# Performance work log

Hardware: AMD Instinct MI355X
Metric: run time of the kernel (lower is better)

## Reference

```python
import jax, jax.numpy as jnp
import numpy as np

ALPHA = 0.5
BETA = 5.0
LOGIT_SCALE = 100.0  # exp(log(100)) -- CLIP's learned logit scale at its clamp value
NUM_CLASSES = 200


def _l2norm(x):
    return x / jnp.linalg.norm(x, axis=-1, keepdims=True)


def setup_inputs() -> dict:
    key = jax.random.key(0)
    k1, k2, k3, k4 = jax.random.split(key, 4)
    img_f = jax.random.normal(k1, (1024, 512), dtype=jnp.float32)
    text_features = jax.random.normal(k2, (200, 512), dtype=jnp.float32)
    keys = jax.random.normal(k3, (50000, 512), dtype=jnp.float32)
    labels = jax.random.randint(k4, (50000,), 0, NUM_CLASSES, dtype=jnp.int64)
    return {"img_f": img_f, "text_features": text_features, "keys": keys, "labels": labels}


def reference(img_f, text_features, keys, labels):
    # encode_image output is L2-normalized in the module; keys were built from
    # normalized image features, text_features are normalized class embeddings.
    q = _l2norm(img_f)            # [B, D]
    t = _l2norm(text_features)    # [C, D]
    k = _l2norm(keys)             # [N, D]

    # CLIP zero-shot branch: scale * q @ t.T -> [B, C]
    z = LOGIT_SCALE * jnp.einsum('bd,cd->bc', q, t)

    # Tip-Adapter cache branch: exp(beta * q @ keys.T) @ one_hot(labels)
    sim = jnp.einsum('bd,nd->bn', q, k)                 # [B, N]
    aff = jnp.exp(BETA * sim)                           # [B, N]
    values = jax.nn.one_hot(labels, NUM_CLASSES, dtype=aff.dtype)  # [N, C]
    c = aff @ values                                    # [B, C]

    return (1.0 - ALPHA) * z + ALPHA * c
```

## Files before the change

### kernel.cpp

```cpp
#include <hip/hip_runtime.h>

#define B_Q    1024
#define D_K    512
#define N_CLS  200
#define N_KEYS 50000
#define N_PAD  50048

typedef __attribute__((ext_vector_type(8))) short bf16x8;
typedef __attribute__((ext_vector_type(4))) float f32x4;

__device__ __forceinline__ float bf2f(unsigned short u) {
  union { unsigned int i; float f; } v; v.i = ((unsigned int)u) << 16; return v.f;
}
__device__ __forceinline__ unsigned short f2bf(float f) {
  union { float f; unsigned int i; } v; v.f = f;
  unsigned int r = v.i + 0x7fffu + ((v.i >> 16) & 1u);
  return (unsigned short)(r >> 16);
}
__device__ __forceinline__ uint4 pack8(const float f[8], float s) {
  uint4 o;
  o.x = (unsigned)f2bf(f[0]*s) | ((unsigned)f2bf(f[1]*s) << 16);
  o.y = (unsigned)f2bf(f[2]*s) | ((unsigned)f2bf(f[3]*s) << 16);
  o.z = (unsigned)f2bf(f[4]*s) | ((unsigned)f2bf(f[5]*s) << 16);
  o.w = (unsigned)f2bf(f[6]*s) | ((unsigned)f2bf(f[7]*s) << 16);
  return o;
}
__device__ __forceinline__ void async_copy16(const void* g, void* lds) {
  __builtin_amdgcn_global_load_lds(
      (const __attribute__((address_space(1))) unsigned int*)g,
      (__attribute__((address_space(3))) unsigned int*)lds, 16, 0, 0);
}

__global__ void k_hist(const int* __restrict__ labels, int* __restrict__ hist) {
  __shared__ int h[N_CLS];
  int t = threadIdx.x;
  if (t < N_CLS) h[t] = 0;
  __syncthreads();
  int n = blockIdx.x * 256 + t;
  if (n < N_KEYS) atomicAdd(&h[labels[n]], 1);
  __syncthreads();
  if (t < N_CLS && h[t]) atomicAdd(&hist[t], h[t]);
}

__global__ void k_scan(const int* __restrict__ hist, int* __restrict__ cursor) {
  __shared__ int s[N_CLS];
  int t = threadIdx.x;
  int v = (t < N_CLS) ? hist[t] : 0;
  if (t < N_CLS) s[t] = v;
  __syncthreads();
  for (int d = 1; d < N_CLS; d <<= 1) {
    int x = 0;
    if (t < N_CLS && t >= d) x = s[t - d];
    __syncthreads();
    if (t < N_CLS) s[t] += x;
    __syncthreads();
  }
  if (t < N_CLS) cursor[t] = s[t] - v;
}

__global__ void k_perm(const int* __restrict__ labels, int* __restrict__ cursor,
                       int* __restrict__ perm, int* __restrict__ cls) {
  __shared__ int lh[N_CLS];
  __shared__ int lbase[N_CLS];
  int t = threadIdx.x;
  if (t < N_CLS) lh[t] = 0;
  __syncthreads();
  int n = blockIdx.x * 256 + t;
  bool valid = (n < N_KEYS);
  int l = 0, lo = 0;
  if (valid) { l = labels[n]; lo = atomicAdd(&lh[l], 1); }
  __syncthreads();
  if (t < N_CLS && lh[t] > 0) lbase[t] = atomicAdd(&cursor[t], lh[t]);
  __syncthreads();
  if (valid) {
    int pos = lbase[l] + lo;
    perm[pos] = n;
    cls[pos] = l;
  } else if (n < N_PAD) {
    cls[n] = N_CLS;
  }
}

__global__ void k_norm2(const float* __restrict__ img, const float* __restrict__ txt,
                        unsigned short* __restrict__ qn, unsigned short* __restrict__ tn) {
  int w = threadIdx.x >> 6, lane = threadIdx.x & 63;
  int row = blockIdx.x * 4 + w;
  const float* in; unsigned short* out; int r;
  if (row < B_Q)                { in = img; out = qn; r = row; }
  else if (row < B_Q + N_CLS)   { in = txt; out = tn; r = row - B_Q; }
  else return;
  const float4* src = (const float4*)(in + (size_t)r * D_K) + lane * 2;
  float4 a = src[0], b = src[1];
  float f[8] = {a.x, a.y, a.z, a.w, b.x, b.y, b.z, b.w};
  float ss = 0.f;
#pragma unroll
  for (int i = 0; i < 8; i++) ss += f[i] * f[i];
#pragma unroll
  for (int d = 1; d < 64; d <<= 1) ss += __shfl_xor(ss, d);
  float rinv = rsqrtf(ss);
  *((uint4*)(out + (size_t)r * D_K) + lane) = pack8(f, rinv);
}

__global__ void k_prep(const float* __restrict__ keys,
                       const int* __restrict__ perm, unsigned short* __restrict__ kn) {
  int w = threadIdx.x >> 6, lane = threadIdx.x & 63;
  int j = blockIdx.x * 4 + w;
  if (j >= N_PAD) return;
  uint4* dst = (uint4*)(kn + (size_t)j * D_K) + lane;
  if (j >= N_KEYS) { *dst = make_uint4(0, 0, 0, 0); return; }
  int n = perm[j];
  const float4* src = (const float4*)(keys + (size_t)n * D_K) + lane * 2;
  float4 a = src[0], b = src[1];
  float f[8] = {a.x, a.y, a.z, a.w, b.x, b.y, b.z, b.w};
  float ss = 0.f;
#pragma unroll
  for (int i = 0; i < 8; i++) ss += f[i] * f[i];
#pragma unroll
  for (int d = 1; d < 64; d <<= 1) ss += __shfl_xor(ss, d);
  float rinv = rsqrtf(ss);
  *dst = pack8(f, rinv);
}

__global__ void k_z(const unsigned short* __restrict__ qn,
                    const unsigned short* __restrict__ tn, float* __restrict__ out) {
  __shared__ float qrow[D_K];
  int t = threadIdx.x, b = blockIdx.x;
  qrow[t]       = bf2f(qn[b * D_K + t]);
  qrow[t + 256] = bf2f(qn[b * D_K + 256 + t]);
  __syncthreads();
  if (t < N_CLS) {
    const uint4* trow = (const uint4*)(tn + (size_t)t * D_K);
    float s = 0.f;
    for (int k8 = 0; k8 < D_K / 8; k8++) {
      uint4 v = trow[k8];
      unsigned short h[8] = {
        (unsigned short)(v.x & 0xffffu), (unsigned short)(v.x >> 16),
        (unsigned short)(v.y & 0xffffu), (unsigned short)(v.y >> 16),
        (unsigned short)(v.z & 0xffffu), (unsigned short)(v.z >> 16),
        (unsigned short)(v.w & 0xffffu), (unsigned short)(v.w >> 16)};
      const float* qp = &qrow[k8 * 8];
#pragma unroll
      for (int i = 0; i < 8; i++) s += bf2f(h[i]) * qp[i];
    }
    out[b * N_CLS + t] = 50.0f * s;
  }
}

__global__ __launch_bounds__(256, 3) void k_main(const unsigned short* __restrict__ qn,
                                                 const unsigned short* __restrict__ kn,
                                                 const int* __restrict__ cls,
                                                 float* __restrict__ out) {
  __shared__ unsigned short As[128 * 64];
  __shared__ unsigned short Bs[128 * 64];
  int t = threadIdx.x;
  int tileB = blockIdx.x, tileN = blockIdx.y;
  int rowB0 = tileB * 128, rowN0 = tileN * 128;

  f32x4 acc[4][4];
#pragma unroll
  for (int i = 0; i < 4; i++)
#pragma unroll
    for (int j = 0; j < 4; j++) acc[i][j] = (f32x4){0.f, 0.f, 0.f, 0.f};

  int lane = t & 63, w = t >> 6;
  int wr = (w >> 1) * 64, wc = (w & 1) * 64;
  int l15 = lane & 15, lq = lane >> 4;
  const int rA = t >> 3;
  const int gsw = ((t & 7) ^ (rA & 7)) * 8;
  const int sw = l15 & 7;

  for (int k0 = 0; k0 < D_K; k0 += 64) {
    __syncthreads();
#pragma unroll
    for (int i = 0; i < 4; i++) {
      int row = i * 32 + rA;
      async_copy16(qn + (size_t)(rowB0 + row) * D_K + k0 + gsw, &As[i * 2048 + t * 8]);
      async_copy16(kn + (size_t)(rowN0 + row) * D_K + k0 + gsw, &Bs[i * 2048 + t * 8]);
    }
    __syncthreads();
#pragma unroll
    for (int ks = 0; ks < 64; ks += 32) {
      bf16x8 af[4], bf[4];
#pragma unroll
      for (int i = 0; i < 4; i++)
        af[i] = *(const bf16x8*)&As[(wr + 16 * i + l15) * 64 + ((((ks >> 3) + lq) ^ sw) * 8)];
#pragma unroll
      for (int j = 0; j < 4; j++)
        bf[j] = *(const bf16x8*)&Bs[(wc + 16 * j + l15) * 64 + ((((ks >> 3) + lq) ^ sw) * 8)];
#pragma unroll
      for (int i = 0; i < 4; i++)
#pragma unroll
        for (int j = 0; j < 4; j++)
          acc[i][j] = __builtin_amdgcn_mfma_f32_16x16x32_bf16(af[i], bf[j], acc[i][j], 0, 0, 0);
    }
  }

#pragma unroll
  for (int i = 0; i < 4; i++)
#pragma unroll
    for (int j = 0; j < 4; j++)
#pragma unroll
      for (int r = 0; r < 4; r++) acc[i][j][r] = __expf(5.0f * acc[i][j][r]);

  int cj[4];
#pragma unroll
  for (int j = 0; j < 4; j++) cj[j] = cls[rowN0 + wc + 16 * j + l15];
  int cseg0 = cls[rowN0 + wc];
  int cseg1 = cls[rowN0 + wc + 63];

  for (int c = cseg0; c <= cseg1; c++) {
    if (c >= N_CLS) break;
#pragma unroll
    for (int i = 0; i < 4; i++) {
      float s0 = 0.f, s1 = 0.f, s2 = 0.f, s3 = 0.f;
#pragma unroll
      for (int j = 0; j < 4; j++) {
        if (cj[j] == c) {
          s0 += acc[i][j][0]; s1 += acc[i][j][1];
          s2 += acc[i][j][2]; s3 += acc[i][j][3];
        }
      }
#pragma unroll
      for (int d = 1; d < 16; d <<= 1) {
        s0 += __shfl_xor(s0, d); s1 += __shfl_xor(s1, d);
        s2 += __shfl_xor(s2, d); s3 += __shfl_xor(s3, d);
      }
      if (l15 == 0) {
        int row = rowB0 + wr + 16 * i + lq * 4;
        float* o = out + (size_t)row * N_CLS + c;
        if (s0 != 0.f) atomicAdd(o + 0 * N_CLS, 0.5f * s0);
        if (s1 != 0.f) atomicAdd(o + 1 * N_CLS, 0.5f * s1);
        if (s2 != 0.f) atomicAdd(o + 2 * N_CLS, 0.5f * s2);
        if (s3 != 0.f) atomicAdd(o + 3 * N_CLS, 0.5f * s3);
      }
    }
  }
}

extern "C" void kernel_launch(void* const* d_in, const int* in_sizes, int n_in,
                              void* d_out, int out_size, void* d_ws, size_t ws_size,
                              hipStream_t stream) {
  (void)in_sizes; (void)n_in; (void)out_size; (void)ws_size;
  const float* img    = (const float*)d_in[0];
  const float* txt    = (const float*)d_in[1];
  const float* keys   = (const float*)d_in[2];
  const int*   labels = (const int*)d_in[3];
  float*       out    = (float*)d_out;

  char* ws = (char*)d_ws;
  unsigned short* qn = (unsigned short*)(ws + 0);
  unsigned short* tn = (unsigned short*)(ws + 1048576);
  unsigned short* kn = (unsigned short*)(ws + 1253376);
  int*  perm   = (int*)(ws + 52502528);
  int*  cls    = (int*)(ws + 52702720);
  int*  hist   = (int*)(ws + 52902912);
  int*  cursor = hist + 256;

  hipMemsetAsync(hist, 0, 256 * sizeof(int), stream);

  k_hist<<<196, 256, 0, stream>>>(labels, hist);
  k_scan<<<1, 256, 0, stream>>>(hist, cursor);
  k_perm<<<196, 256, 0, stream>>>(labels, cursor, perm, cls);
  k_norm2<<<(B_Q + N_CLS + 3) / 4, 256, 0, stream>>>(img, txt, qn, tn);
  k_prep<<<N_PAD / 4, 256, 0, stream>>>(keys, perm, kn);
  k_z<<<B_Q, 256, 0, stream>>>(qn, tn, out);
  k_main<<<dim3(B_Q / 128, N_PAD / 128), 256, 0, stream>>>(qn, kn, cls, out);
}
```

Before: 309.3 us.

## Fuse normalization kernels, fold text logits into main GEMM, double-buffer LDS

```diff
diff --git a/kernel.cpp b/kernel.cpp
--- a/kernel.cpp
+++ b/kernel.cpp
@@ -5,13 +5,12 @@
 #define N_CLS  200
 #define N_KEYS 50000
 #define N_PAD  50048
+#define N_EXT  (N_PAD + 256)
+#define N_ZT   (N_PAD / 128)
 
 typedef __attribute__((ext_vector_type(8))) short bf16x8;
 typedef __attribute__((ext_vector_type(4))) float f32x4;
 
-__device__ __forceinline__ float bf2f(unsigned short u) {
-  union { unsigned int i; float f; } v; v.i = ((unsigned int)u) << 16; return v.f;
-}
 __device__ __forceinline__ unsigned short f2bf(float f) {
   union { float f; unsigned int i; } v; v.f = f;
   unsigned int r = v.i + 0x7fffu + ((v.i >> 16) & 1u);
@@ -59,7 +58,7 @@
 }
 
 __global__ void k_perm(const int* __restrict__ labels, int* __restrict__ cursor,
-                       int* __restrict__ perm, int* __restrict__ cls) {
+                       int* __restrict__ dest) {
   __shared__ int lh[N_CLS];
   __shared__ int lbase[N_CLS];
   int t = threadIdx.x;
@@ -72,25 +71,41 @@
   __syncthreads();
   if (t < N_CLS && lh[t] > 0) lbase[t] = atomicAdd(&cursor[t], lh[t]);
   __syncthreads();
-  if (valid) {
-    int pos = lbase[l] + lo;
-    perm[pos] = n;
-    cls[pos] = l;
-  } else if (n < N_PAD) {
-    cls[n] = N_CLS;
-  }
-}
-
-__global__ void k_norm2(const float* __restrict__ img, const float* __restrict__ txt,
-                        unsigned short* __restrict__ qn, unsigned short* __restrict__ tn) {
+  if (valid) dest[n] = lbase[l] + lo;
+}
+
+__global__ void k_prep2(const float* __restrict__ keys, const float* __restrict__ img,
+                        const float* __restrict__ txt, const int* __restrict__ labels,
+                        const int* __restrict__ dest, unsigned short* __restrict__ qn,
+                        unsigned short* __restrict__ kn, int* __restrict__ cls) {
   int w = threadIdx.x >> 6, lane = threadIdx.x & 63;
   int row = blockIdx.x * 4 + w;
-  const float* in; unsigned short* out; int r;
-  if (row < B_Q)                { in = img; out = qn; r = row; }
-  else if (row < B_Q + N_CLS)   { in = txt; out = tn; r = row - B_Q; }
-  else return;
-  const float4* src = (const float4*)(in + (size_t)r * D_K) + lane * 2;
-  float4 a = src[0], b = src[1];
+  const float* src; unsigned short* dst; int r;
+  if (row < N_PAD) {
+    if (row >= N_KEYS) {
+      *((uint4*)(kn + (size_t)row * D_K) + lane) = make_uint4(0, 0, 0, 0);
+      if (lane == 0) cls[row] = N_CLS;
+      return;
+    }
+    int d = dest[row];
+    if (lane == 0) cls[d] = labels[row];
+    src = keys + (size_t)row * D_K;
+    dst = kn + (size_t)d * D_K;
+  } else if (row < N_PAD + B_Q) {
+    r = row - N_PAD;
+    src = img + (size_t)r * D_K;
+    dst = qn + (size_t)r * D_K;
+  } else if (row < N_PAD + B_Q + N_CLS) {
+    r = row - N_PAD - B_Q;
+    src = txt + (size_t)r * D_K;
+    dst = kn + (size_t)(N_PAD + r) * D_K;
+  } else if (row < N_PAD + B_Q + N_CLS + 56) {
+    r = N_PAD + N_CLS + (row - N_PAD - B_Q - N_CLS);
+    *((uint4*)(kn + (size_t)r * D_K) + lane) = make_uint4(0, 0, 0, 0);
+    return;
+  } else return;
+  const float4* s4 = (const float4*)src + lane * 2;
+  float4 a = s4[0], b = s4[1];
   float f[8] = {a.x, a.y, a.z, a.w, b.x, b.y, b.z, b.w};
   float ss = 0.f;
 #pragma unroll
@@ -98,60 +113,15 @@
 #pragma unroll
   for (int d = 1; d < 64; d <<= 1) ss += __shfl_xor(ss, d);
   float rinv = rsqrtf(ss);
-  *((uint4*)(out + (size_t)r * D_K) + lane) = pack8(f, rinv);
-}
-
-__global__ void k_prep(const float* __restrict__ keys,
-                       const int* __restrict__ perm, unsigned short* __restrict__ kn) {
-  int w = threadIdx.x >> 6, lane = threadIdx.x & 63;
-  int j = blockIdx.x * 4 + w;
-  if (j >= N_PAD) return;
-  uint4* dst = (uint4*)(kn + (size_t)j * D_K) + lane;
-  if (j >= N_KEYS) { *dst = make_uint4(0, 0, 0, 0); return; }
-  int n = perm[j];
-  const float4* src = (const float4*)(keys + (size_t)n * D_K) + lane * 2;
-  float4 a = src[0], b = src[1];
-  float f[8] = {a.x, a.y, a.z, a.w, b.x, b.y, b.z, b.w};
-  float ss = 0.f;
-#pragma unroll
-  for (int i = 0; i < 8; i++) ss += f[i] * f[i];
-#pragma unroll
-  for (int d = 1; d < 64; d <<= 1) ss += __shfl_xor(ss, d);
-  float rinv = rsqrtf(ss);
-  *dst = pack8(f, rinv);
-}
-
-__global__ void k_z(const unsigned short* __restrict__ qn,
-                    const unsigned short* __restrict__ tn, float* __restrict__ out) {
-  __shared__ float qrow[D_K];
-  int t = threadIdx.x, b = blockIdx.x;
-  qrow[t]       = bf2f(qn[b * D_K + t]);
-  qrow[t + 256] = bf2f(qn[b * D_K + 256 + t]);
-  __syncthreads();
-  if (t < N_CLS) {
-    const uint4* trow = (const uint4*)(tn + (size_t)t * D_K);
-    float s = 0.f;
-    for (int k8 = 0; k8 < D_K / 8; k8++) {
-      uint4 v = trow[k8];
-      unsigned short h[8] = {
-        (unsigned short)(v.x & 0xffffu), (unsigned short)(v.x >> 16),
-        (unsigned short)(v.y & 0xffffu), (unsigned short)(v.y >> 16),
-        (unsigned short)(v.z & 0xffffu), (unsigned short)(v.z >> 16),
-        (unsigned short)(v.w & 0xffffu), (unsigned short)(v.w >> 16)};
-      const float* qp = &qrow[k8 * 8];
-#pragma unroll
-      for (int i = 0; i < 8; i++) s += bf2f(h[i]) * qp[i];
-    }
-    out[b * N_CLS + t] = 50.0f * s;
-  }
-}
-
-__global__ __launch_bounds__(256, 3) void k_main(const unsigned short* __restrict__ qn,
+  *((uint4*)dst + lane) = pack8(f, rinv);
+}
+
+__global__ __launch_bounds__(256, 2) void k_main(const unsigned short* __restrict__ qn,
                                                  const unsigned short* __restrict__ kn,
                                                  const int* __restrict__ cls,
                                                  float* __restrict__ out) {
-  __shared__ unsigned short As[128 * 64];
-  __shared__ unsigned short Bs[128 * 64];
+  __shared__ unsigned short As[2][128 * 64];
+  __shared__ unsigned short Bs[2][128 * 64];
   int t = threadIdx.x;
   int tileB = blockIdx.x, tileN = blockIdx.y;
   int rowB0 = tileB * 128, rowN0 = tileN * 128;
@@ -169,30 +139,57 @@
   const int gsw = ((t & 7) ^ (rA & 7)) * 8;
   const int sw = l15 & 7;
 
-  for (int k0 = 0; k0 < D_K; k0 += 64) {
+#pragma unroll
+  for (int i = 0; i < 4; i++) {
+    int row = i * 32 + rA;
+    async_copy16(qn + (size_t)(rowB0 + row) * D_K + gsw, &As[0][i * 2048 + t * 8]);
+    async_copy16(kn + (size_t)(rowN0 + row) * D_K + gsw, &Bs[0][i * 2048 + t * 8]);
+  }
+
+  for (int kt = 0; kt < 8; kt++) {
+    int cur = kt & 1;
     __syncthreads();
-#pragma unroll
-    for (int i = 0; i < 4; i++) {
-      int row = i * 32 + rA;
-      async_copy16(qn + (size_t)(rowB0 + row) * D_K + k0 + gsw, &As[i * 2048 + t * 8]);
-      async_copy16(kn + (size_t)(rowN0 + row) * D_K + k0 + gsw, &Bs[i * 2048 + t * 8]);
-    }
-    __syncthreads();
+    if (kt < 7) {
+      int nxt = cur ^ 1, k0 = (kt + 1) * 64;
+#pragma unroll
+      for (int i = 0; i < 4; i++) {
+        int row = i * 32 + rA;
+        async_copy16(qn + (size_t)(rowB0 + row) * D_K + k0 + gsw, &As[nxt][i * 2048 + t * 8]);
+        async_copy16(kn + (size_t)(rowN0 + row) * D_K + k0 + gsw, &Bs[nxt][i * 2048 + t * 8]);
+      }
+    }
 #pragma unroll
     for (int ks = 0; ks < 64; ks += 32) {
       bf16x8 af[4], bf[4];
 #pragma unroll
       for (int i = 0; i < 4; i++)
-        af[i] = *(const bf16x8*)&As[(wr + 16 * i + l15) * 64 + ((((ks >> 3) + lq) ^ sw) * 8)];
+        af[i] = *(const bf16x8*)&As[cur][(wr + 16 * i + l15) * 64 + ((((ks >> 3) + lq) ^ sw) * 8)];
 #pragma unroll
       for (int j = 0; j < 4; j++)
-        bf[j] = *(const bf16x8*)&Bs[(wc + 16 * j + l15) * 64 + ((((ks >> 3) + lq) ^ sw) * 8)];
+        bf[j] = *(const bf16x8*)&Bs[cur][(wc + 16 * j + l15) * 64 + ((((ks >> 3) + lq) ^ sw) * 8)];
 #pragma unroll
       for (int i = 0; i < 4; i++)
 #pragma unroll
         for (int j = 0; j < 4; j++)
           acc[i][j] = __builtin_amdgcn_mfma_f32_16x16x32_bf16(af[i], bf[j], acc[i][j], 0, 0, 0);
     }
+  }
+
+  if (tileN >= N_ZT) {
+#pragma unroll
+    for (int i = 0; i < 4; i++)
+#pragma unroll
+      for (int j = 0; j < 4; j++) {
+        int col = rowN0 + wc + 16 * j + l15 - N_PAD;
+        if (col < N_CLS) {
+#pragma unroll
+          for (int r = 0; r < 4; r++) {
+            int row = rowB0 + wr + 16 * i + lq * 4 + r;
+            atomicAdd(out + (size_t)row * N_CLS + col, 50.0f * acc[i][j][r]);
+          }
+        }
+      }
+    return;
   }
 
 #pragma unroll
@@ -249,20 +246,19 @@
 
   char* ws = (char*)d_ws;
   unsigned short* qn = (unsigned short*)(ws + 0);
-  unsigned short* tn = (unsigned short*)(ws + 1048576);
-  unsigned short* kn = (unsigned short*)(ws + 1253376);
-  int*  perm   = (int*)(ws + 52502528);
-  int*  cls    = (int*)(ws + 52702720);
-  int*  hist   = (int*)(ws + 52902912);
-  int*  cursor = hist + 256;
+  unsigned short* kn = (unsigned short*)(ws + 1048576);
+  int*  dest   = (int*)(ws + 52559872);
+  int*  cls    = (int*)(ws + 52760064);
+  int*  hist   = (int*)(ws + 52960256);
+  int*  cursor = (int*)(ws + 52961280);
 
   hipMemsetAsync(hist, 0, 256 * sizeof(int), stream);
+  hipMemsetAsync(out, 0, (size_t)B_Q * N_CLS * sizeof(float), stream);
 
   k_hist<<<196, 256, 0, stream>>>(labels, hist);
   k_scan<<<1, 256, 0, stream>>>(hist, cursor);
-  k_perm<<<196, 256, 0, stream>>>(labels, cursor, perm, cls);
-  k_norm2<<<(B_Q + N_CLS + 3) / 4, 256, 0, stream>>>(img, txt, qn, tn);
-  k_prep<<<N_PAD / 4, 256, 0, stream>>>(keys, perm, kn);
-  k_z<<<B_Q, 256, 0, stream>>>(qn, tn, out);
-  k_main<<<dim3(B_Q / 128, N_PAD / 128), 256, 0, stream>>>(qn, kn, cls, out);
-}
+  k_perm<<<196, 256, 0, stream>>>(labels, cursor, dest);
+  k_prep2<<<(N_PAD + B_Q + N_CLS + 56 + 3) / 4, 256, 0, stream>>>(
+      keys, img, txt, labels, dest, qn, kn, cls);
+  k_main<<<dim3(B_Q / 128, N_ZT + 2), 256, 0, stream>>>(qn, kn, cls, out);
+}
```

Result: faster. 297.4 us (-3.8%).
